# Kernel optimization log

Hardware: AMD Instinct MI355X
Metric: run time of the kernel (lower is better)

The kernel has to match this reference:

```python
import jax, jax.numpy as jnp
from jax import lax
import numpy as np

B, T, NAG, MTASK = 8, 32, 50, 100  # batch, timesteps, n agents, m tasks
MTOP, NNB, L, H = 10, 10, 5, 512   # M top tasks, N neighbors (must equal M), L, hidden_dim
IN_DIM = NNB * MTOP * L + NNB * MTASK + NNB + NNB * MTOP  # 1610


def setup_inputs() -> dict:
    key = jax.random.key(0)
    ks = jax.random.split(key, 8)
    return {
        "beta": jax.random.normal(ks[0], (B, T, NAG, MTASK, L), dtype=jnp.float32),
        "actions_onehot": jax.random.uniform(ks[1], (B, T, NAG, MTASK), dtype=jnp.float32),
        "power_states": jax.random.normal(ks[2], (B, T, NAG), dtype=jnp.float32),
        "prev_assigns": jax.random.randint(ks[3], (B, T, NAG), 0, MTASK, dtype=jnp.int32),
        "W1": jax.random.normal(ks[4], (IN_DIM, H), dtype=jnp.float32) * 0.02,
        "b1": jnp.zeros((H,), jnp.float32),
        "W2": jax.random.normal(ks[5], (H, H), dtype=jnp.float32) * 0.02,
        "b2": jnp.zeros((H,), jnp.float32),
        "W3": jax.random.normal(ks[6], (H, MTOP + 1), dtype=jnp.float32) * 0.02,
        "b3": jnp.zeros((MTOP + 1,), jnp.float32),
    }


def _gather_agents(x, nb_flat):
    # x: [B,T,n,...]; nb_flat: [B,T,n*N] int -> [B,T,n,N,...]
    idx = nb_flat.reshape(B, T, NAG * NNB, *([1] * (x.ndim - 3)))
    out = jnp.take_along_axis(x, idx, axis=2)
    return out.reshape(B, T, NAG, NNB, *x.shape[3:])


def reference(beta, actions_onehot, power_states, prev_assigns, W1, b1, W2, b2, W3, b3):
    total_beta = beta.sum(-1)                              # [B,T,n,m]
    _, tasks = lax.top_k(total_beta, MTOP)                 # [B,T,n,M] top tasks per agent

    # benefit of agent a's best among agent i's top-M tasks: [B,T,i,a]
    tb_g = jnp.take_along_axis(total_beta, tasks.reshape(B, T, 1, NAG * MTOP), axis=3)
    best = tb_g.reshape(B, T, NAG, NAG, MTOP).max(-1)      # [B,T,a,i]
    best = best.transpose(0, 1, 3, 2)                      # [B,T,i,a]
    best = jnp.where(jnp.eye(NAG, dtype=bool), -jnp.inf, best)
    _, neighbors = lax.top_k(best, NNB)                    # [B,T,n,N]
    nb_flat = neighbors.reshape(B, T, NAG * NNB)

    # beta features: beta[b,t,nb(i,j),tasks(i,k),l] flattened in (M,N,L) order
    beta_nb = _gather_agents(beta, nb_flat)                # [B,T,n,N,m,L]
    beta_sel = jnp.take_along_axis(beta_nb, tasks[:, :, :, None, :, None], axis=4)  # [B,T,n,N,M,L]
    beta_feat = beta_sel.transpose(0, 1, 2, 4, 3, 5).reshape(B, T, NAG, NNB * MTOP * L)

    act_feat = _gather_agents(actions_onehot, nb_flat).reshape(B, T, NAG, NNB * MTASK)
    pow_feat = _gather_agents(power_states, nb_flat)       # [B,T,n,N]

    pa_nb = _gather_agents(prev_assigns, nb_flat)          # [B,T,n,N] int
    # one_hot(prev_assign)[task] == (prev_assign == task); flattened (M,N) order
    prev_feat = (tasks[:, :, :, :, None] == pa_nb[:, :, :, None, :]).astype(beta.dtype)
    prev_feat = prev_feat.reshape(B, T, NAG, MTOP * NNB)

    inputs = jnp.concatenate([beta_feat, act_feat, pow_feat, prev_feat], axis=-1)  # [B,T,n,1610]
    x = jax.nn.relu(inputs @ W1 + b1)
    x = jax.nn.relu(x @ W2 + b2)
    q = x @ W3 + b3                                        # [B,T,n,M+1]
    return q
```

## Files before the change

### kernel.cpp

```cpp
#include <hip/hip_runtime.h>
#include <math.h>

#define NB 8
#define NT 32
#define NAG 50
#define MTASK 100
#define MTOP 10
#define NNB 10
#define LDIM 5
#define HDIM 512
#define INDIM 1610
#define KP1 1664
#define NKT1 (KP1/32)
#define NKT2 (HDIM/32)
#define NROWS (NB*NT*NAG)
#define NOUT (MTOP+1)

typedef float f32x4 __attribute__((ext_vector_type(4)));
typedef _Float16 f16;
typedef _Float16 f16x8 __attribute__((ext_vector_type(8)));

__device__ __forceinline__ void gload16(const void* g, void* l) {
    __builtin_amdgcn_global_load_lds(
        (__attribute__((address_space(1))) void*)(g),
        (__attribute__((address_space(3))) void*)(l), 16, 0, 0);
}


__global__ __launch_bounds__(256) void k_topk(const float* __restrict__ beta,
                                              float* __restrict__ total_beta,
                                              int* __restrict__ tasks) {
    int wid = threadIdx.x >> 6, lane = threadIdx.x & 63;
    int row = blockIdx.x * 4 + wid;
    const float* bp = beta + (size_t)row * MTASK * LDIM;
    float v1, v2 = -INFINITY;
    {
        const float* p = bp + lane * LDIM;
        v1 = p[0] + p[1] + p[2] + p[3] + p[4];
        total_beta[(size_t)row * MTASK + lane] = v1;
    }
    if (lane + 64 < MTASK) {
        const float* p = bp + (lane + 64) * LDIM;
        v2 = p[0] + p[1] + p[2] + p[3] + p[4];
        total_beta[(size_t)row * MTASK + lane + 64] = v2;
    }
    for (int k = 0; k < MTOP; ++k) {
        float v; int idx;
        if (v1 >= v2) { v = v1; idx = lane; } else { v = v2; idx = lane + 64; }
        #pragma unroll
        for (int m = 1; m < 64; m <<= 1) {
            float vo = __shfl_xor(v, m, 64);
            int io = __shfl_xor(idx, m, 64);
            if (vo > v || (vo == v && io < idx)) { v = vo; idx = io; }
        }
        if (lane == 0) tasks[row * MTOP + k] = idx;
        if (idx == lane) v1 = -INFINITY;
        else if (idx == lane + 64) v2 = -INFINITY;
    }
}

__global__ __launch_bounds__(256) void k_nbrs(const float* __restrict__ total_beta,
                                              const int* __restrict__ tasks,
                                              int* __restrict__ neighbors) {
    int wid = threadIdx.x >> 6, lane = threadIdx.x & 63;
    int row = blockIdx.x * 4 + wid;
    int bt = row / NAG, i = row - bt * NAG;
    int tk[MTOP];
    #pragma unroll
    for (int k = 0; k < MTOP; ++k) tk[k] = tasks[row * MTOP + k];
    float v1 = -INFINITY;
    if (lane < NAG) {
        const float* tba = total_beta + ((size_t)bt * NAG + lane) * MTASK;
        float mx = -INFINITY;
        #pragma unroll
        for (int k = 0; k < MTOP; ++k) mx = fmaxf(mx, tba[tk[k]]);
        v1 = (lane == i) ? -INFINITY : mx;
    }
    for (int k = 0; k < NNB; ++k) {
        float v = v1; int idx = lane;
        #pragma unroll
        for (int m = 1; m < 64; m <<= 1) {
            float vo = __shfl_xor(v, m, 64);
            int io = __shfl_xor(idx, m, 64);
            if (vo > v || (vo == v && io < idx)) { v = vo; idx = io; }
        }
        if (lane == 0) neighbors[row * NNB + k] = idx;
        if (idx == lane) v1 = -INFINITY;
    }
}

__global__ __launch_bounds__(256) void k_build_inputs(
    const float* __restrict__ beta, const float* __restrict__ actions,
    const float* __restrict__ power, const int* __restrict__ prev,
    const int* __restrict__ tasks, const int* __restrict__ neighbors,
    f16* __restrict__ A) {
    int b = blockIdx.x;
    int t = threadIdx.x;
    __shared__ int tkv[8][MTOP], nbv[8][NNB], pav[8][NNB];
    __shared__ float pwv[8][NNB];
    __shared__ float fbuf[8][500];
    __shared__ float abuf[8][1004];
    if (t < 80) {
        int lr = t / 10, j = t - lr * 10;
        int row = b * 8 + lr;
        int bt = row / NAG;
        int nbj = neighbors[row * NNB + j];
        nbv[lr][j] = nbj;
        pav[lr][j] = prev[bt * NAG + nbj];
        pwv[lr][j] = power[bt * NAG + nbj];
        tkv[lr][j] = tasks[row * MTOP + j];
    }
    __syncthreads();
    int row0 = b * 8;
    #pragma unroll
    for (int it = 0; it < 4; ++it) {
        int idx = t + it * 256;
        if (idx < 800) {
            int l = idx / 100, p = idx - l * 100;
            int k = p / 10, j = p - k * 10;
            int row = row0 + l;
            int bt = row / NAG;
            const float* src = beta + ((size_t)(bt * NAG + nbv[l][j]) * MTASK
                                       + tkv[l][k]) * LDIM;
            int c0 = k * 50 + j * 5;
            #pragma unroll
            for (int i = 0; i < 5; ++i) fbuf[l][c0 + i] = src[i];
        }
    }
    #pragma unroll
    for (int it = 0; it < 8; ++it) {
        int idx = t + it * 256;
        if (idx < 2000) {
            int l = idx / 250, v = idx - l * 250;
            int j = v / 25, q = v - j * 25;
            int row = row0 + l;
            int bt = row / NAG;
            f32x4 a = *(const f32x4*)&actions[(size_t)(bt * NAG + nbv[l][j]) * MTASK + q * 4];
            *(f32x4*)&abuf[l][j * 100 + q * 4] = a;
        }
    }
    __syncthreads();
    int l = t & 7, og = t >> 3;
    int row = row0 + l;
    int rb = row >> 6, rlo = row & 63;
    #pragma unroll
    for (int s = 0; s < 7; ++s) {
        int o = og + 32 * s;
        if (o < 208) {
            f16 h8[8];
            #pragma unroll
            for (int e = 0; e < 8; ++e) {
                int c = o * 8 + e;
                float f;
                if (c < 500) {
                    f = fbuf[l][c];
                } else if (c < 1500) {
                    f = abuf[l][c - 500];
                } else if (c < 1510) {
                    f = pwv[l][c - 1500];
                } else if (c < 1610) {
                    int r2 = c - 1510, k = r2 / NNB, j = r2 - k * NNB;
                    f = (tkv[l][k] == pav[l][j]) ? 1.f : 0.f;
                } else {
                    f = 0.f;
                }
                h8[e] = (f16)f;
            }
            size_t off = ((size_t)rb * 208 + o) * 512 + rlo * 8;
            *(f16x8*)&A[off] = *(f16x8*)h8;
        }
    }
}

__global__ __launch_bounds__(256) void k_prep_wt(const float* __restrict__ W1,
                                                 const float* __restrict__ W2,
                                                 f16* __restrict__ T1,
                                                 f16* __restrict__ T2) {
    int bx = blockIdx.x, n0 = blockIdx.y * 64;
    const float* W; f16* T; int K, NKT, kp0;
    if (bx < KP1 / 64) { W = W1; T = T1; K = INDIM; NKT = NKT1; kp0 = bx * 64; }
    else               { W = W2; T = T2; K = HDIM;  NKT = NKT2; kp0 = (bx - KP1 / 64) * 64; }
    __shared__ float lds[64][65];
    int t = threadIdx.x;
    int cc = t & 63, r0 = t >> 6;
    #pragma unroll
    for (int i = 0; i < 16; ++i) {
        int rr = r0 + i * 4;
        int kp = kp0 + rr;
        lds[rr][cc] = (kp < K) ? W[(size_t)kp * HDIM + n0 + cc] : 0.f;
    }
    __syncthreads();
    int nblk = n0 >> 6;
    #pragma unroll
    for (int s = 0; s < 2; ++s) {
        int o = t + s * 256;
        int rn = o & 63, ko = o >> 6;
        int kp = kp0 + ko * 8;
        int kt = kp >> 5, kc = (kp >> 3) & 3;
        f16 h8[8];
        #pragma unroll
        for (int e = 0; e < 8; ++e) h8[e] = (f16)lds[ko * 8 + e][rn];
        size_t off = ((size_t)(nblk * NKT + kt) * 4 + kc) * 512 + rn * 8;
        *(f16x8*)&T[off] = *(f16x8*)h8;
    }
}

template<int NKT, int MODE>
__global__ __launch_bounds__(256, 4) void k_gemm(
    const f16* __restrict__ Ap, const f16* __restrict__ Bp,
    const float* __restrict__ bias, f16* __restrict__ C,
    const float* __restrict__ W3, float* __restrict__ qpart) {
    constexpr int SMEM = (MODE == 0) ? 34048 : 39680;
    __shared__ __align__(16) char smem[SMEM];
    f16* sA = (f16*)smem;
    f16* sB = (f16*)(smem + 8192);
    int tid = threadIdx.x, wid = tid >> 6, lane = tid & 63;
    int id = blockIdx.x;
    int swz = (id & 7) * 100 + (id >> 3);
    int nt = swz & 3, mt = swz >> 2;

    auto stage = [&](int kk, int buf) {
        #pragma unroll
        for (int j = 0; j < 3; ++j) {
            int seg = wid + 4 * j;
            if (seg < 4) {
                gload16(Ap + ((size_t)(mt * NKT + kk) * 4 + seg) * 512 + lane * 8,
                        sA + buf * 2048 + seg * 512);
            } else {
                int s = seg - 4, q = s >> 2, kc = s & 3;
                gload16(Bp + ((size_t)((2 * nt + q) * NKT + kk) * 4 + kc) * 512 + lane * 8,
                        sB + buf * 4096 + (kc * 128 + q * 64) * 8);
            }
        }
    };

    int wr = wid >> 1, wc = wid & 1;
    int lrow = lane & 15, lk = lane >> 4;
    f32x4 acc[2][4] = {};

    stage(0, 0);
    for (int kk = 0; kk < NKT; ++kk) {
        int buf = kk & 1;
        __syncthreads();
        if (kk + 1 < NKT) stage(kk + 1, buf ^ 1);
        f16x8 a[2], bh[4];
        #pragma unroll
        for (int i = 0; i < 2; ++i)
            a[i] = *(const f16x8*)(sA + buf * 2048 + (lk * 64 + wr * 32 + i * 16 + lrow) * 8);
        #pragma unroll
        for (int j = 0; j < 4; ++j)
            bh[j] = *(const f16x8*)(sB + buf * 4096 + (lk * 128 + wc * 64 + j * 16 + lrow) * 8);
        #pragma unroll
        for (int i = 0; i < 2; ++i)
            #pragma unroll
            for (int j = 0; j < 4; ++j)
                acc[i][j] = __builtin_amdgcn_mfma_f32_16x16x32_f16(a[i], bh[j], acc[i][j], 0, 0, 0);
    }

    __syncthreads();
    float* sE = (float*)smem;
    #pragma unroll
    for (int i = 0; i < 2; ++i)
        #pragma unroll
        for (int j = 0; j < 4; ++j)
            #pragma unroll
            for (int r = 0; r < 4; ++r)
                sE[(wr * 32 + i * 16 + lk * 4 + r) * 133 + wc * 64 + j * 16 + lrow] = acc[i][j][r];

    if constexpr (MODE == 0) {
        __syncthreads();
        int l2 = tid & 63, og2 = tid >> 6;
        #pragma unroll
        for (int s2 = 0; s2 < 4; ++s2) {
            int o = og2 + 4 * s2;
            int n0 = nt * 128 + o * 8;
            f32x4 v0 = *(f32x4*)&sE[l2 * 133 + o * 8];
            f32x4 v1 = *(f32x4*)&sE[l2 * 133 + o * 8 + 4];
            f32x4 bb0 = *(const f32x4*)&bias[n0];
            f32x4 bb1 = *(const f32x4*)&bias[n0 + 4];
            f16 h8[8];
            #pragma unroll
            for (int i = 0; i < 4; ++i) {
                h8[i] = (f16)fmaxf(v0[i] + bb0[i], 0.f);
                h8[4 + i] = (f16)fmaxf(v1[i] + bb1[i], 0.f);
            }
            size_t off = ((size_t)mt * 64 + nt * 16 + o) * 512 + l2 * 8;
            *(f16x8*)&C[off] = *(f16x8*)h8;
        }
    } else {
        float* W3s = (float*)(smem + 34048);
        for (int i = tid; i < 128 * NOUT; i += 256)
            W3s[i] = W3[nt * 128 * NOUT + i];
        __syncthreads();
        int row = tid >> 2, seg = tid & 3;
        float a11[NOUT];
        #pragma unroll
        for (int n = 0; n < NOUT; ++n) a11[n] = 0.f;
        #pragma unroll
        for (int c32 = 0; c32 < 32; ++c32) {
            int col = seg + 4 * c32;
            float h = fmaxf(sE[row * 133 + col] + bias[nt * 128 + col], 0.f);
            const float* w = W3s + col * NOUT;
            #pragma unroll
            for (int n = 0; n < NOUT; ++n) a11[n] += h * w[n];
        }
        #pragma unroll
        for (int d = 2; d >= 1; d >>= 1)
            #pragma unroll
            for (int n = 0; n < NOUT; ++n) a11[n] += __shfl_down(a11[n], d, 64);
        if (seg == 0) {
            int grow = mt * 64 + row;
            #pragma unroll
            for (int n = 0; n < NOUT; ++n)
                qpart[(size_t)nt * NROWS * NOUT + (size_t)grow * NOUT + n] = a11[n];
        }
    }
}

__global__ __launch_bounds__(256) void k_qreduce(const float* __restrict__ qp,
                                                 const float* __restrict__ b3,
                                                 float* __restrict__ out) {
    int i = blockIdx.x * 256 + threadIdx.x;
    if (i < NROWS * NOUT) {
        int n = i % NOUT;
        const size_t P = (size_t)NROWS * NOUT;
        out[i] = b3[n] + qp[i] + qp[i + P] + qp[i + 2 * P] + qp[i + 3 * P];
    }
}

extern "C" void kernel_launch(void* const* d_in, const int* in_sizes, int n_in,
                              void* d_out, int out_size, void* d_ws, size_t ws_size,
                              hipStream_t stream) {
    const float* beta    = (const float*)d_in[0];
    const float* actions = (const float*)d_in[1];
    const float* power   = (const float*)d_in[2];
    const int*   prev    = (const int*)d_in[3];
    const float* W1      = (const float*)d_in[4];
    const float* b1      = (const float*)d_in[5];
    const float* W2      = (const float*)d_in[6];
    const float* b2      = (const float*)d_in[7];
    const float* W3      = (const float*)d_in[8];
    const float* b3      = (const float*)d_in[9];
    float* out = (float*)d_out;

    char* ws = (char*)d_ws;
    size_t off = 0;
    auto alloc = [&](size_t bytes) { void* p = ws + off; off += (bytes + 255) & ~(size_t)255; return p; };
    float* total_beta = (float*)alloc((size_t)NROWS * MTASK * 4);
    int*   tasks      = (int*)  alloc((size_t)NROWS * MTOP * 4);
    int*   neighbors  = (int*)  alloc((size_t)NROWS * NNB * 4);
    f16*   A    = (f16*)alloc((size_t)NROWS * KP1 * 2);
    f16*   W1t  = (f16*)alloc((size_t)HDIM * KP1 * 2);
    f16*   W2t  = (f16*)alloc((size_t)HDIM * HDIM * 2);
    f16*   h1   = (f16*)alloc((size_t)NROWS * HDIM * 2);
    float* qpart = (float*)alloc((size_t)4 * NROWS * NOUT * 4);

    k_topk<<<NROWS / 4, 256, 0, stream>>>(beta, total_beta, tasks);
    k_nbrs<<<NROWS / 4, 256, 0, stream>>>(total_beta, tasks, neighbors);
    k_build_inputs<<<NROWS / 8, 256, 0, stream>>>(beta, actions, power, prev, tasks,
                                                  neighbors, A);
    {
        dim3 gp(KP1 / 64 + HDIM / 64, HDIM / 64);
        k_prep_wt<<<gp, 256, 0, stream>>>(W1, W2, W1t, W2t);
    }
    k_gemm<NKT1, 0><<<800, 256, 0, stream>>>(A, W1t, b1, h1, nullptr, nullptr);
    k_gemm<NKT2, 1><<<800, 256, 0, stream>>>(h1, W2t, b2, nullptr, W3, qpart);
    k_qreduce<<<(NROWS * NOUT + 255) / 256, 256, 0, stream>>>(qpart, b3, out);
}
```

Measured before the change: 144.0 us.

## Merge weight prep into top-k kernel and load GEMM A operand directly to registers

The weight transpose/convert kernel is folded into the top-k kernel as extra blocks, which removes one launch and lets the two independent jobs run concurrently. In both GEMMs the A tile is no longer staged through LDS. Each wave now loads its A fragments straight from global memory into registers, and only B still goes through the async LDS double buffer. This removes LDS traffic and staging instructions for A, but the A loads are now synchronous global loads issued inside the k-loop with no prefetch, so their latency may be exposed.

```diff
diff --git a/kernel.cpp b/kernel.cpp
--- a/kernel.cpp
+++ b/kernel.cpp
@@ -15,6 +15,9 @@
 #define NKT2 (HDIM/32)
 #define NROWS (NB*NT*NAG)
 #define NOUT (MTOP+1)
+#define NTOPKB (NROWS/4)
+#define NPREPX (KP1/64 + HDIM/64)
+#define NPREPB (NPREPX * (HDIM/64))
 
 typedef float f32x4 __attribute__((ext_vector_type(4)));
 typedef _Float16 f16;
@@ -27,35 +30,68 @@
 }
 
 
-__global__ __launch_bounds__(256) void k_topk(const float* __restrict__ beta,
-                                              float* __restrict__ total_beta,
-                                              int* __restrict__ tasks) {
-    int wid = threadIdx.x >> 6, lane = threadIdx.x & 63;
-    int row = blockIdx.x * 4 + wid;
-    const float* bp = beta + (size_t)row * MTASK * LDIM;
-    float v1, v2 = -INFINITY;
-    {
-        const float* p = bp + lane * LDIM;
-        v1 = p[0] + p[1] + p[2] + p[3] + p[4];
-        total_beta[(size_t)row * MTASK + lane] = v1;
-    }
-    if (lane + 64 < MTASK) {
-        const float* p = bp + (lane + 64) * LDIM;
-        v2 = p[0] + p[1] + p[2] + p[3] + p[4];
-        total_beta[(size_t)row * MTASK + lane + 64] = v2;
-    }
-    for (int k = 0; k < MTOP; ++k) {
-        float v; int idx;
-        if (v1 >= v2) { v = v1; idx = lane; } else { v = v2; idx = lane + 64; }
-        #pragma unroll
-        for (int m = 1; m < 64; m <<= 1) {
-            float vo = __shfl_xor(v, m, 64);
-            int io = __shfl_xor(idx, m, 64);
-            if (vo > v || (vo == v && io < idx)) { v = vo; idx = io; }
-        }
-        if (lane == 0) tasks[row * MTOP + k] = idx;
-        if (idx == lane) v1 = -INFINITY;
-        else if (idx == lane + 64) v2 = -INFINITY;
+__global__ __launch_bounds__(256) void k_topk_prep(
+    const float* __restrict__ beta, float* __restrict__ total_beta,
+    int* __restrict__ tasks,
+    const float* __restrict__ W1, const float* __restrict__ W2,
+    f16* __restrict__ T1, f16* __restrict__ T2) {
+    __shared__ float lds[64][65];
+    if (blockIdx.x < NTOPKB) {
+        int wid = threadIdx.x >> 6, lane = threadIdx.x & 63;
+        int row = blockIdx.x * 4 + wid;
+        const float* bp = beta + (size_t)row * MTASK * LDIM;
+        float v1, v2 = -INFINITY;
+        {
+            const float* p = bp + lane * LDIM;
+            v1 = p[0] + p[1] + p[2] + p[3] + p[4];
+            total_beta[(size_t)row * MTASK + lane] = v1;
+        }
+        if (lane + 64 < MTASK) {
+            const float* p = bp + (lane + 64) * LDIM;
+            v2 = p[0] + p[1] + p[2] + p[3] + p[4];
+            total_beta[(size_t)row * MTASK + lane + 64] = v2;
+        }
+        for (int k = 0; k < MTOP; ++k) {
+            float v; int idx;
+            if (v1 >= v2) { v = v1; idx = lane; } else { v = v2; idx = lane + 64; }
+            #pragma unroll
+            for (int m = 1; m < 64; m <<= 1) {
+                float vo = __shfl_xor(v, m, 64);
+                int io = __shfl_xor(idx, m, 64);
+                if (vo > v || (vo == v && io < idx)) { v = vo; idx = io; }
+            }
+            if (lane == 0) tasks[row * MTOP + k] = idx;
+            if (idx == lane) v1 = -INFINITY;
+            else if (idx == lane + 64) v2 = -INFINITY;
+        }
+    } else {
+        int pb = blockIdx.x - NTOPKB;
+        int bx = pb % NPREPX, n0 = (pb / NPREPX) * 64;
+        const float* W; f16* T; int K, NKT, kp0;
+        if (bx < KP1 / 64) { W = W1; T = T1; K = INDIM; NKT = NKT1; kp0 = bx * 64; }
+        else               { W = W2; T = T2; K = HDIM;  NKT = NKT2; kp0 = (bx - KP1 / 64) * 64; }
+        int t = threadIdx.x;
+        int cc = t & 63, r0 = t >> 6;
+        #pragma unroll
+        for (int i = 0; i < 16; ++i) {
+            int rr = r0 + i * 4;
+            int kp = kp0 + rr;
+            lds[rr][cc] = (kp < K) ? W[(size_t)kp * HDIM + n0 + cc] : 0.f;
+        }
+        __syncthreads();
+        int nblk = n0 >> 6;
+        #pragma unroll
+        for (int s = 0; s < 2; ++s) {
+            int o = t + s * 256;
+            int rn = o & 63, ko = o >> 6;
+            int kp = kp0 + ko * 8;
+            int kt = kp >> 5, kc = (kp >> 3) & 3;
+            f16 h8[8];
+            #pragma unroll
+            for (int e = 0; e < 8; ++e) h8[e] = (f16)lds[ko * 8 + e][rn];
+            size_t off = ((size_t)(nblk * NKT + kt) * 4 + kc) * 512 + rn * 8;
+            *(f16x8*)&T[off] = *(f16x8*)h8;
+        }
     }
 }
 
@@ -172,39 +208,6 @@
     }
 }
 
-__global__ __launch_bounds__(256) void k_prep_wt(const float* __restrict__ W1,
-                                                 const float* __restrict__ W2,
-                                                 f16* __restrict__ T1,
-                                                 f16* __restrict__ T2) {
-    int bx = blockIdx.x, n0 = blockIdx.y * 64;
-    const float* W; f16* T; int K, NKT, kp0;
-    if (bx < KP1 / 64) { W = W1; T = T1; K = INDIM; NKT = NKT1; kp0 = bx * 64; }
-    else               { W = W2; T = T2; K = HDIM;  NKT = NKT2; kp0 = (bx - KP1 / 64) * 64; }
-    __shared__ float lds[64][65];
-    int t = threadIdx.x;
-    int cc = t & 63, r0 = t >> 6;
-    #pragma unroll
-    for (int i = 0; i < 16; ++i) {
-        int rr = r0 + i * 4;
-        int kp = kp0 + rr;
-        lds[rr][cc] = (kp < K) ? W[(size_t)kp * HDIM + n0 + cc] : 0.f;
-    }
-    __syncthreads();
-    int nblk = n0 >> 6;
-    #pragma unroll
-    for (int s = 0; s < 2; ++s) {
-        int o = t + s * 256;
-        int rn = o & 63, ko = o >> 6;
-        int kp = kp0 + ko * 8;
-        int kt = kp >> 5, kc = (kp >> 3) & 3;
-        f16 h8[8];
-        #pragma unroll
-        for (int e = 0; e < 8; ++e) h8[e] = (f16)lds[ko * 8 + e][rn];
-        size_t off = ((size_t)(nblk * NKT + kt) * 4 + kc) * 512 + rn * 8;
-        *(f16x8*)&T[off] = *(f16x8*)h8;
-    }
-}
-
 template<int NKT, int MODE>
 __global__ __launch_bounds__(256, 4) void k_gemm(
     const f16* __restrict__ Ap, const f16* __restrict__ Bp,
@@ -212,8 +215,7 @@
     const float* __restrict__ W3, float* __restrict__ qpart) {
     constexpr int SMEM = (MODE == 0) ? 34048 : 39680;
     __shared__ __align__(16) char smem[SMEM];
-    f16* sA = (f16*)smem;
-    f16* sB = (f16*)(smem + 8192);
+    f16* sB = (f16*)smem;
     int tid = threadIdx.x, wid = tid >> 6, lane = tid & 63;
     int id = blockIdx.x;
     int swz = (id & 7) * 100 + (id >> 3);
@@ -221,16 +223,11 @@
 
     auto stage = [&](int kk, int buf) {
         #pragma unroll
-        for (int j = 0; j < 3; ++j) {
+        for (int j = 0; j < 2; ++j) {
             int seg = wid + 4 * j;
-            if (seg < 4) {
-                gload16(Ap + ((size_t)(mt * NKT + kk) * 4 + seg) * 512 + lane * 8,
-                        sA + buf * 2048 + seg * 512);
-            } else {
-                int s = seg - 4, q = s >> 2, kc = s & 3;
-                gload16(Bp + ((size_t)((2 * nt + q) * NKT + kk) * 4 + kc) * 512 + lane * 8,
-                        sB + buf * 4096 + (kc * 128 + q * 64) * 8);
-            }
+            int q = seg >> 2, kc = seg & 3;
+            gload16(Bp + ((size_t)((2 * nt + q) * NKT + kk) * 4 + kc) * 512 + lane * 8,
+                    sB + buf * 4096 + (kc * 128 + q * 64) * 8);
         }
     };
 
@@ -242,19 +239,19 @@
     for (int kk = 0; kk < NKT; ++kk) {
         int buf = kk & 1;
         __syncthreads();
+        size_t abase = ((size_t)(mt * NKT + kk) * 4 + lk) * 512 + (wr * 32 + lrow) * 8;
+        f16x8 a0 = *(const f16x8*)(Ap + abase);
+        f16x8 a1 = *(const f16x8*)(Ap + abase + 128);
         if (kk + 1 < NKT) stage(kk + 1, buf ^ 1);
-        f16x8 a[2], bh[4];
-        #pragma unroll
-        for (int i = 0; i < 2; ++i)
-            a[i] = *(const f16x8*)(sA + buf * 2048 + (lk * 64 + wr * 32 + i * 16 + lrow) * 8);
+        f16x8 bh[4];
         #pragma unroll
         for (int j = 0; j < 4; ++j)
             bh[j] = *(const f16x8*)(sB + buf * 4096 + (lk * 128 + wc * 64 + j * 16 + lrow) * 8);
         #pragma unroll
-        for (int i = 0; i < 2; ++i)
-            #pragma unroll
-            for (int j = 0; j < 4; ++j)
-                acc[i][j] = __builtin_amdgcn_mfma_f32_16x16x32_f16(a[i], bh[j], acc[i][j], 0, 0, 0);
+        for (int j = 0; j < 4; ++j) {
+            acc[0][j] = __builtin_amdgcn_mfma_f32_16x16x32_f16(a0, bh[j], acc[0][j], 0, 0, 0);
+            acc[1][j] = __builtin_amdgcn_mfma_f32_16x16x32_f16(a1, bh[j], acc[1][j], 0, 0, 0);
+        }
     }
 
     __syncthreads();
@@ -355,14 +352,11 @@
     f16*   h1   = (f16*)alloc((size_t)NROWS * HDIM * 2);
     float* qpart = (float*)alloc((size_t)4 * NROWS * NOUT * 4);
 
-    k_topk<<<NROWS / 4, 256, 0, stream>>>(beta, total_beta, tasks);
+    k_topk_prep<<<NTOPKB + NPREPB, 256, 0, stream>>>(beta, total_beta, tasks,
+                                                     W1, W2, W1t, W2t);
     k_nbrs<<<NROWS / 4, 256, 0, stream>>>(total_beta, tasks, neighbors);
     k_build_inputs<<<NROWS / 8, 256, 0, stream>>>(beta, actions, power, prev, tasks,
                                                   neighbors, A);
-    {
-        dim3 gp(KP1 / 64 + HDIM / 64, HDIM / 64);
-        k_prep_wt<<<gp, 256, 0, stream>>>(W1, W2, W1t, W2t);
-    }
     k_gemm<NKT1, 0><<<800, 256, 0, stream>>>(A, W1t, b1, h1, nullptr, nullptr);
     k_gemm<NKT2, 1><<<800, 256, 0, stream>>>(h1, W2t, b2, nullptr, W3, qpart);
     k_qreduce<<<(NROWS * NOUT + 255) / 256, 256, 0, stream>>>(qpart, b3, out);
```

Result: no change. 141.8 us, median of 2 (-1.5%).
